# Performance work log

Hardware: AMD Instinct MI355X
Metric: run time of the kernel (lower is better)

The kernel has to match this reference:

```python
import jax, jax.numpy as jnp
import numpy as np
import math

B, S, D, H = 16, 1024, 768, 12
Dh = D // H  # 64


def setup_inputs() -> dict:
    key = jax.random.key(0)
    ks = jax.random.split(key, 9)
    scale = 1.0 / math.sqrt(D)
    X = jax.random.normal(ks[0], (B, S, D), dtype=jnp.float32)
    # Per-head Q/K/V projections stacked along head dim: [H, D, Dh]
    Wq = jax.random.normal(ks[1], (H, D, Dh), dtype=jnp.float32) * scale
    Wk = jax.random.normal(ks[2], (H, D, Dh), dtype=jnp.float32) * scale
    Wv = jax.random.normal(ks[3], (H, D, Dh), dtype=jnp.float32) * scale
    bq = jax.random.normal(ks[4], (H, Dh), dtype=jnp.float32) * scale
    bk = jax.random.normal(ks[5], (H, Dh), dtype=jnp.float32) * scale
    bv = jax.random.normal(ks[6], (H, Dh), dtype=jnp.float32) * scale
    Wo = jax.random.normal(ks[7], (D, D), dtype=jnp.float32) * scale
    bo = jax.random.normal(ks[8], (D,), dtype=jnp.float32) * scale
    return {"X": X, "Wq": Wq, "bq": bq, "Wk": Wk, "bk": bk,
            "Wv": Wv, "bv": bv, "Wo": Wo, "bo": bo}


def reference(X, Wq, bq, Wk, bk, Wv, bv, Wo, bo):
    # Batched multi-head QKV projections (equivalent to the per-head Linear loop).
    Q = jnp.einsum('bsd,hde->bhse', X, Wq) + bq[None, :, None, :]
    K = jnp.einsum('bsd,hde->bhse', X, Wk) + bk[None, :, None, :]
    V = jnp.einsum('bsd,hde->bhse', X, Wv) + bv[None, :, None, :]
    scores = jnp.einsum('bhse,bhte->bhst', Q, K) / jnp.sqrt(jnp.float32(Dh))
    A = jax.nn.softmax(scores, axis=-1)            # [B,H,S,S]
    O = jnp.einsum('bhst,bhte->bhse', A, V)        # [B,H,S,Dh]
    # Concat heads along feature dim (matches torch cat order: head 0 first).
    msa = jnp.transpose(O, (0, 2, 1, 3)).reshape(B, S, D)
    return msa @ Wo + bo
```

## Files before the change

kernel.cpp:

```cpp
#include <hip/hip_runtime.h>
#include <hip/hip_bf16.h>

#define BB 16
#define SS 1024
#define DD 768
#define HH 12
#define DH 64

typedef short short8 __attribute__((ext_vector_type(8)));
typedef float f32x4 __attribute__((ext_vector_type(4)));

__device__ inline float b2f(unsigned short v) {
    union { unsigned int u; float f; } x; x.u = ((unsigned int)v) << 16; return x.f;
}
__device__ inline unsigned short f2b(float f) {
    unsigned int u = __float_as_uint(f);
    u += 0x7FFFu + ((u >> 16) & 1u);
    return (unsigned short)(u >> 16);
}
__device__ inline unsigned int pk2(float a, float b) {
    __hip_bfloat162 h = __float22bfloat162_rn(make_float2(a, b));
    return *(unsigned int*)&h;
}
__device__ inline void cvt8(unsigned short* dst, const float* src) {
    const float4 f0 = *(const float4*)src;
    const float4 f1 = *(const float4*)(src + 4);
    unsigned short t[8] = {f2b(f0.x), f2b(f0.y), f2b(f0.z), f2b(f0.w),
                           f2b(f1.x), f2b(f1.y), f2b(f1.z), f2b(f1.w)};
    *(uint4*)dst = *(const uint4*)t;
}
__device__ __forceinline__ void async16(const void* g, void* l) {
    __builtin_amdgcn_global_load_lds(
        (const __attribute__((address_space(1))) void*)g,
        (__attribute__((address_space(3))) void*)l, 16, 0, 0);
}

__global__ __launch_bounds__(256) void detect_kernel(const unsigned short* __restrict__ X,
                                                     int* __restrict__ flag) {
    __shared__ int s;
    if (threadIdx.x == 0) s = 0;
    __syncthreads();
    int c = 0;
    for (int i = threadIdx.x; i < 16384; i += 256) {
        unsigned short v = X[i];
        if ((v & 0x7FFFu) >= 0x7F80u) c = 1;
    }
    if (c) s = 1;
    __syncthreads();
    if (threadIdx.x == 0) flag[0] = s;
}

__global__ __launch_bounds__(256) void prep_all(
    const void* __restrict__ Xv,
    const void* __restrict__ Wqv, const void* __restrict__ bqv,
    const void* __restrict__ Wkv, const void* __restrict__ bkv,
    const void* __restrict__ Wvv, const void* __restrict__ bvv,
    const void* __restrict__ Wov, const void* __restrict__ bov,
    const int* __restrict__ flag,
    unsigned short* __restrict__ Xb, unsigned short* __restrict__ Wc,
    unsigned short* __restrict__ Wot, unsigned short* __restrict__ bc,
    float* __restrict__ bo32)
{
    __shared__ unsigned short Ls[64][72];
    const int dt = *flag;
    const int u = threadIdx.x;
    const int bx = blockIdx.x;

    if (bx < 6144) {
        size_t base = ((size_t)bx * 256 + u) * 8;
        if (dt) cvt8(Xb + base, (const float*)Xv + base);
        else    *(uint4*)(Xb + base) = *(const uint4*)((const unsigned short*)Xv + base);
        return;
    }
    if (bx < 6720) {
        const int idx = bx - 6144;
        const int kt = idx % 12;
        const int y  = idx / 12;
        const int rk = u >> 2;
        const int e0 = (u & 3) * 16;

        const void* src; size_t srcBase;
        unsigned short* dst; int drow;
        if (y < 36) {
            int z = y / 12, h = y % 12;
            src = (z == 0) ? Wqv : (z == 1) ? Wkv : Wvv;
            srcBase = ((size_t)h * DD + kt * 64 + rk) * DH;
            dst = Wc; drow = z * 768 + h * 64;
        } else {
            int nt = y - 36;
            src = Wov;
            srcBase = (size_t)(kt * 64 + rk) * DD + nt * 64;
            dst = Wot; drow = nt * 64;
        }
#pragma unroll
        for (int ii = 0; ii < 2; ++ii) {
            int e = e0 + ii * 8;
            if (dt) {
                const float* p = (const float*)src + srcBase + e;
                float4 a = *(const float4*)p, b = *(const float4*)(p + 4);
                float v[8] = {a.x, a.y, a.z, a.w, b.x, b.y, b.z, b.w};
#pragma unroll
                for (int j = 0; j < 8; ++j) Ls[e + j][rk] = f2b(v[j]);
            } else {
                union { uint4 v; unsigned short s[8]; } t;
                t.v = *(const uint4*)((const unsigned short*)src + srcBase + e);
#pragma unroll
                for (int j = 0; j < 8; ++j) Ls[e + j][rk] = t.s[j];
            }
        }
        __syncthreads();
        const int e = u >> 2, q = u & 3;
#pragma unroll
        for (int ii = 0; ii < 2; ++ii) {
            int kk = q * 16 + ii * 8;
            *(uint4*)(dst + (size_t)(drow + e) * DD + kt * 64 + kk) = *(const uint4*)(&Ls[e][kk]);
        }
        return;
    }
    for (int n = u; n < 2304; n += 256) {
        int z = n / 768, i = n % 768;
        const void* b = (z == 0) ? bqv : (z == 1) ? bkv : bvv;
        bc[n] = dt ? f2b(((const float*)b)[i]) : ((const unsigned short*)b)[i];
    }
    for (int n = u; n < 768; n += 256)
        bo32[n] = dt ? ((const float*)bov)[n] : b2f(((const unsigned short*)bov)[n]);
}

__global__ __launch_bounds__(256) void qkv_gemm(
    const unsigned short* __restrict__ Xb,
    const unsigned short* __restrict__ Wc,
    const unsigned short* __restrict__ bc,
    unsigned short* __restrict__ Qb, unsigned short* __restrict__ Kb,
    unsigned short* __restrict__ Vtb)
{
    __shared__ __align__(16) unsigned short lds[17408];
    unsigned short* As = lds;
    unsigned short* Bs = lds + 128 * 64;

    const int u = threadIdx.x;
    const int lane = u & 63, w = u >> 6;
    const int ln = lane & 15, quad = lane >> 4;
    const int wm = w & 1, wn = w >> 1;

    const int nt0 = blockIdx.x;
    const int m0  = blockIdx.y << 7;
    const int n0  = nt0 << 7;
    const int z   = nt0 / 6;
    const int hpair = (nt0 % 6) * 2;

    const int rA = w * 32 + (lane >> 3);
    const int c8 = (((lane & 7) ^ (lane >> 3)) * 8);

    f32x4 acc[4][4];
#pragma unroll
    for (int i = 0; i < 4; ++i)
#pragma unroll
        for (int j = 0; j < 4; ++j) acc[i][j] = (f32x4){0.f, 0.f, 0.f, 0.f};

    const unsigned short* Ag = Xb + (size_t)(m0 + rA) * DD + c8;
    const unsigned short* Bg = Wc + (size_t)(n0 + rA) * DD + c8;
    unsigned short* lA0 = As + w * 2048;
    unsigned short* lB0 = Bs + w * 2048;

    for (int kb = 0; kb < 12; ++kb) {
        const int k0 = kb * 64;
        if (kb) __syncthreads();
#pragma unroll
        for (int j = 0; j < 4; ++j) {
            async16(Ag + (size_t)j * 8 * DD + k0, lA0 + j * 512);
            async16(Bg + (size_t)j * 8 * DD + k0, lB0 + j * 512);
        }
        __syncthreads();
#pragma unroll
        for (int kh = 0; kh < 2; ++kh) {
            const int sx = ((kh * 4 + quad) ^ (ln & 7)) * 8;
            short8 af[4], bf[4];
#pragma unroll
            for (int t = 0; t < 4; ++t) {
                af[t] = *(const short8*)(As + (wm * 64 + t * 16 + ln) * 64 + sx);
                bf[t] = *(const short8*)(Bs + (wn * 64 + t * 16 + ln) * 64 + sx);
            }
#pragma unroll
            for (int mt = 0; mt < 4; ++mt)
#pragma unroll
                for (int nt = 0; nt < 4; ++nt)
                    acc[mt][nt] = __builtin_amdgcn_mfma_f32_16x16x32_bf16(af[mt], bf[nt], acc[mt][nt], 0, 0, 0);
        }
    }

    float bias[4];
#pragma unroll
    for (int nt = 0; nt < 4; ++nt) bias[nt] = b2f(bc[n0 + wn * 64 + nt * 16 + ln]);

    const int b = m0 >> 10;
    if (z < 2) {
        unsigned short* O = (z == 0) ? Qb : Kb;
        const float sc = (z == 0) ? 0.180336880111120f : 1.0f;
        const int h = hpair + wn;
        const int sb = (m0 & 1023) + wm * 64;
#pragma unroll
        for (int mt = 0; mt < 4; ++mt)
#pragma unroll
            for (int r = 0; r < 4; ++r) {
                int s = sb + mt * 16 + quad * 4 + r;
                size_t rowo = ((size_t)(b * HH + h) * SS + s) * DH;
#pragma unroll
                for (int nt = 0; nt < 4; ++nt)
                    O[rowo + nt * 16 + ln] = f2b((acc[mt][nt][r] + bias[nt]) * sc);
            }
    } else {
        __syncthreads();
#pragma unroll
        for (int mt = 0; mt < 4; ++mt)
#pragma unroll
            for (int nt = 0; nt < 4; ++nt)
#pragma unroll
                for (int r = 0; r < 4; ++r)
                    lds[(wn * 64 + nt * 16 + ln) * 136 + wm * 64 + mt * 16 + quad * 4 + r] =
                        f2b(acc[mt][nt][r] + bias[nt]);
        __syncthreads();
        const int cc = u >> 1, half = u & 1;
        const int h = hpair + (cc >> 6), e = cc & 63;
        const int sb = (m0 & 1023) + half * 64;
        unsigned short* dst = Vtb + ((size_t)(b * HH + h) * DH + e) * SS + sb;
        const unsigned short* srcp = lds + cc * 136 + half * 64;
#pragma unroll
        for (int i = 0; i < 8; ++i)
            *(uint4*)(dst + i * 8) = *(const uint4*)(srcp + i * 8);
    }
}

__global__ __launch_bounds__(256, 6) void attn_kernel(
    const unsigned short* __restrict__ Kb,
    const unsigned short* __restrict__ Vtb,
    unsigned short* __restrict__ Qb)
{
    __shared__ __align__(16) unsigned short QPs[64][72];
    __shared__ __align__(16) unsigned short Ks[4096];
    __shared__ __align__(16) unsigned short Vs[4096];

    const int u = threadIdx.x;
    const int s0 = blockIdx.x << 6;
    const int bh = blockIdx.y;

    const int lane = u & 63, w = u >> 6;
    const int ln = lane & 15, quad = lane >> 4;

    unsigned short* Qg = Qb + ((size_t)bh * SS + s0) * DH;
    const unsigned short* Kg = Kb + (size_t)bh * SS * DH;
    const unsigned short* Vg = Vtb + (size_t)bh * DH * SS;

    const int xrow = u >> 3, xch = u & 7;
#pragma unroll
    for (int p = 0; p < 2; ++p) {
        int r2 = xrow + 32 * p;
        *(uint4*)(&QPs[r2][xch * 8]) = *(const uint4*)(Qg + r2 * DH + xch * 8);
    }
    __syncthreads();
    short8 qf0 = *(const short8*)(&QPs[16 * w + ln][quad * 8]);
    short8 qf1 = *(const short8*)(&QPs[16 * w + ln][32 + quad * 8]);

    short8 ones;
#pragma unroll
    for (int i = 0; i < 8; ++i) ones[i] = (short)0x3F80;

    f32x4 acc_o[4];
#pragma unroll
    for (int i = 0; i < 4; ++i) acc_o[i] = (f32x4){0.f, 0.f, 0.f, 0.f};
    f32x4 acc_l = (f32x4){0.f, 0.f, 0.f, 0.f};

    const int srow = lane >> 3;
    const int cg8  = ((lane & 7) ^ srow) * 8;
    const unsigned short* kp0 = Kg + (size_t)((w * 2 + 0) * 8 + srow) * DH + cg8;
    const unsigned short* kp1 = Kg + (size_t)((w * 2 + 1) * 8 + srow) * DH + cg8;
    const unsigned short* vp0 = Vg + (size_t)((w * 2 + 0) * 8 + srow) * SS + cg8;
    const unsigned short* vp1 = Vg + (size_t)((w * 2 + 1) * 8 + srow) * SS + cg8;
    unsigned short* lk0 = Ks + (w * 2 + 0) * 512;
    unsigned short* lk1 = Ks + (w * 2 + 1) * 512;
    unsigned short* lv0 = Vs + (w * 2 + 0) * 512;
    unsigned short* lv1 = Vs + (w * 2 + 1) * 512;

    const unsigned short* kb0 = Ks + ln * 64 + ((quad) ^ (ln & 7)) * 8;
    const unsigned short* kb1 = Ks + ln * 64 + ((4 + quad) ^ (ln & 7)) * 8;
    const unsigned short* vb0 = Vs + ln * 64 + ((quad) ^ (ln & 7)) * 8;
    const unsigned short* vb1 = Vs + ln * 64 + ((4 + quad) ^ (ln & 7)) * 8;
    unsigned short* psw = &QPs[16 * w + ln][quad * 4];
    const unsigned short* psr0 = &QPs[16 * w + ln][quad * 8];
    const unsigned short* psr1 = &QPs[16 * w + ln][32 + quad * 8];

    for (int kt = 0; kt < 16; ++kt) {
        __syncthreads();
        async16(kp0, lk0); async16(kp1, lk1);
        async16(vp0, lv0); async16(vp1, lv1);
        kp0 += 64 * DH; kp1 += 64 * DH; vp0 += 64; vp1 += 64;
        __syncthreads();

        f32x4 acc_s[4];
#pragma unroll
        for (int nt = 0; nt < 4; ++nt) {
            short8 kf0 = *(const short8*)(kb0 + nt * 1024);
            short8 kf1 = *(const short8*)(kb1 + nt * 1024);
            f32x4 zz = (f32x4){0.f, 0.f, 0.f, 0.f};
            zz = __builtin_amdgcn_mfma_f32_16x16x32_bf16(kf0, qf0, zz, 0, 0, 0);
            zz = __builtin_amdgcn_mfma_f32_16x16x32_bf16(kf1, qf1, zz, 0, 0, 0);
            acc_s[nt] = zz;
        }

#pragma unroll
        for (int nt = 0; nt < 4; ++nt) {
            uint2 pw;
            pw.x = pk2(exp2f(acc_s[nt][0]), exp2f(acc_s[nt][1]));
            pw.y = pk2(exp2f(acc_s[nt][2]), exp2f(acc_s[nt][3]));
            *(uint2*)(psw + nt * 16) = pw;
        }

        short8 pf0 = *(const short8*)psr0;
        short8 pf1 = *(const short8*)psr1;
        acc_l = __builtin_amdgcn_mfma_f32_16x16x32_bf16(pf0, ones, acc_l, 0, 0, 0);
        acc_l = __builtin_amdgcn_mfma_f32_16x16x32_bf16(pf1, ones, acc_l, 0, 0, 0);
#pragma unroll
        for (int nt = 0; nt < 4; ++nt) {
            short8 vf0 = *(const short8*)(vb0 + nt * 1024);
            short8 vf1 = *(const short8*)(vb1 + nt * 1024);
            acc_o[nt] = __builtin_amdgcn_mfma_f32_16x16x32_bf16(pf0, vf0, acc_o[nt], 0, 0, 0);
            acc_o[nt] = __builtin_amdgcn_mfma_f32_16x16x32_bf16(pf1, vf1, acc_o[nt], 0, 0, 0);
        }
    }

    float inv[4];
#pragma unroll
    for (int r = 0; r < 4; ++r) inv[r] = 1.f / acc_l[r];
#pragma unroll
    for (int nt = 0; nt < 4; ++nt)
#pragma unroll
        for (int r = 0; r < 4; ++r) {
            int row = 16 * w + quad * 4 + r;
            Qg[row * DH + nt * 16 + ln] = f2b(acc_o[nt][r] * inv[r]);
        }
}

__global__ __launch_bounds__(256) void oproj_gemm(
    const unsigned short* __restrict__ Ob,
    const unsigned short* __restrict__ Wot,
    const float* __restrict__ bo32,
    float* __restrict__ out)
{
    __shared__ __align__(16) unsigned short lds[128 * 128];
    unsigned short* As = lds;
    unsigned short* Bs = lds + 128 * 64;

    const int u = threadIdx.x;
    const int lane = u & 63, w = u >> 6;
    const int ln = lane & 15, quad = lane >> 4;
    const int wm = w & 1, wn = w >> 1;

    const int n0 = blockIdx.x << 7;
    const int m0 = blockIdx.y << 7;
    const int b = m0 >> 10, s0t = m0 & 1023;

    const int rA = w * 32 + (lane >> 3);
    const int c8 = (((lane & 7) ^ (lane >> 3)) * 8);

    f32x4 acc[4][4];
#pragma unroll
    for (int i = 0; i < 4; ++i)
#pragma unroll
        for (int j = 0; j < 4; ++j) acc[i][j] = (f32x4){0.f, 0.f, 0.f, 0.f};

    const unsigned short* Bg = Wot + (size_t)(n0 + rA) * DD + c8;
    unsigned short* lA0 = As + w * 2048;
    unsigned short* lB0 = Bs + w * 2048;

    for (int kb = 0; kb < 12; ++kb) {
        if (kb) __syncthreads();
        const unsigned short* Ag = Ob + ((size_t)(b * HH + kb) * SS + s0t + rA) * DH + c8;
#pragma unroll
        for (int j = 0; j < 4; ++j) {
            async16(Ag + (size_t)j * 8 * DH, lA0 + j * 512);
            async16(Bg + (size_t)j * 8 * DD + kb * 64, lB0 + j * 512);
        }
        __syncthreads();
#pragma unroll
        for (int kh = 0; kh < 2; ++kh) {
            const int sx = ((kh * 4 + quad) ^ (ln & 7)) * 8;
            short8 af[4], bf[4];
#pragma unroll
            for (int t = 0; t < 4; ++t) {
                af[t] = *(const short8*)(As + (wm * 64 + t * 16 + ln) * 64 + sx);
                bf[t] = *(const short8*)(Bs + (wn * 64 + t * 16 + ln) * 64 + sx);
            }
#pragma unroll
            for (int mt = 0; mt < 4; ++mt)
#pragma unroll
                for (int nt = 0; nt < 4; ++nt)
                    acc[mt][nt] = __builtin_amdgcn_mfma_f32_16x16x32_bf16(af[mt], bf[nt], acc[mt][nt], 0, 0, 0);
        }
    }

    float bias[4];
#pragma unroll
    for (int nt = 0; nt < 4; ++nt) bias[nt] = bo32[n0 + wn * 64 + nt * 16 + ln];
#pragma unroll
    for (int mt = 0; mt < 4; ++mt)
#pragma unroll
        for (int r = 0; r < 4; ++r) {
            int m = m0 + wm * 64 + mt * 16 + quad * 4 + r;
            float* orow = out + (size_t)m * DD + n0 + wn * 64;
#pragma unroll
            for (int nt = 0; nt < 4; ++nt)
                orow[nt * 16 + ln] = acc[mt][nt][r] + bias[nt];
        }
}

extern "C" void kernel_launch(void* const* d_in, const int* in_sizes, int n_in,
                              void* d_out, int out_size, void* d_ws, size_t ws_size,
                              hipStream_t stream)
{
    const void* X  = d_in[0];
    const void* Wq = d_in[1];
    const void* bq = d_in[2];
    const void* Wk = d_in[3];
    const void* bk = d_in[4];
    const void* Wv = d_in[5];
    const void* bv = d_in[6];
    const void* Wo = d_in[7];
    const void* bo = d_in[8];
    float* out = (float*)d_out;

    const size_t NE = (size_t)BB * HH * SS * DH;
    char* p = (char*)d_ws;
    int* flag = (int*)p;                 p += 256;
    unsigned short* Qb  = (unsigned short*)p;  p += NE * 2;
    unsigned short* Kb  = (unsigned short*)p;  p += NE * 2;
    unsigned short* Vtb = (unsigned short*)p;  p += NE * 2;
    unsigned short* Xb  = (unsigned short*)p;  p += (size_t)BB * SS * DD * 2;
    unsigned short* Wc  = (unsigned short*)p;  p += (size_t)3 * DD * DD * 2;
    unsigned short* Wot = (unsigned short*)p;  p += (size_t)DD * DD * 2;
    unsigned short* bcb = (unsigned short*)p;  p += 4608;
    float* bo32 = (float*)p;                   p += 3072;

    detect_kernel<<<1, 256, 0, stream>>>((const unsigned short*)X, flag);
    prep_all<<<6721, 256, 0, stream>>>(X, Wq, bq, Wk, bk, Wv, bv, Wo, bo, flag,
                                       Xb, Wc, Wot, bcb, bo32);
    qkv_gemm<<<dim3(18, 128), 256, 0, stream>>>(Xb, Wc, bcb, Qb, Kb, Vtb);
    attn_kernel<<<dim3(16, 192), 256, 0, stream>>>(Kb, Vtb, Qb);
    oproj_gemm<<<dim3(6, 128), 256, 0, stream>>>(Qb, Wot, bo32, out);
}
```

Measured before the change: 326.2 us.

## Process 128 query rows per attention block to reuse K/V tiles

The attention kernel now handles 128 query rows per block (two 64-row sub-blocks per wave) instead of 64, halving the grid and halving K/V tile loads per query. Q is loaded with async global-to-LDS copies into a swizzled layout, P is written back through the same swizzle, and exp2f is replaced with the hardware exp2 builtin. The cost is more registers and LDS per block, with the occupancy hint lowered from 6 to 4 and fewer blocks in flight.

```diff
diff --git a/kernel.cpp b/kernel.cpp
--- a/kernel.cpp
+++ b/kernel.cpp
@@ -21,6 +21,13 @@
 __device__ inline unsigned int pk2(float a, float b) {
     __hip_bfloat162 h = __float22bfloat162_rn(make_float2(a, b));
     return *(unsigned int*)&h;
+}
+__device__ __forceinline__ float fast_exp2(float x) {
+#if __has_builtin(__builtin_amdgcn_exp2f)
+    return __builtin_amdgcn_exp2f(x);
+#else
+    return exp2f(x);
+#endif
 }
 __device__ inline void cvt8(unsigned short* dst, const float* src) {
     const float4 f0 = *(const float4*)src;
@@ -230,17 +237,17 @@
     }
 }
 
-__global__ __launch_bounds__(256, 6) void attn_kernel(
+__global__ __launch_bounds__(256, 4) void attn_kernel(
     const unsigned short* __restrict__ Kb,
     const unsigned short* __restrict__ Vtb,
     unsigned short* __restrict__ Qb)
 {
-    __shared__ __align__(16) unsigned short QPs[64][72];
+    __shared__ __align__(16) unsigned short QPs[8192];
     __shared__ __align__(16) unsigned short Ks[4096];
     __shared__ __align__(16) unsigned short Vs[4096];
 
     const int u = threadIdx.x;
-    const int s0 = blockIdx.x << 6;
+    const int s0 = blockIdx.x << 7;
     const int bh = blockIdx.y;
 
     const int lane = u & 63, w = u >> 6;
@@ -250,27 +257,38 @@
     const unsigned short* Kg = Kb + (size_t)bh * SS * DH;
     const unsigned short* Vg = Vtb + (size_t)bh * DH * SS;
 
-    const int xrow = u >> 3, xch = u & 7;
-#pragma unroll
-    for (int p = 0; p < 2; ++p) {
-        int r2 = xrow + 32 * p;
-        *(uint4*)(&QPs[r2][xch * 8]) = *(const uint4*)(Qg + r2 * DH + xch * 8);
-    }
-    __syncthreads();
-    short8 qf0 = *(const short8*)(&QPs[16 * w + ln][quad * 8]);
-    short8 qf1 = *(const short8*)(&QPs[16 * w + ln][32 + quad * 8]);
-
-    short8 ones;
-#pragma unroll
-    for (int i = 0; i < 8; ++i) ones[i] = (short)0x3F80;
-
-    f32x4 acc_o[4];
-#pragma unroll
-    for (int i = 0; i < 4; ++i) acc_o[i] = (f32x4){0.f, 0.f, 0.f, 0.f};
-    f32x4 acc_l = (f32x4){0.f, 0.f, 0.f, 0.f};
-
     const int srow = lane >> 3;
     const int cg8  = ((lane & 7) ^ srow) * 8;
+
+#pragma unroll
+    for (int j = 0; j < 4; ++j) {
+        const int r0 = (w * 4 + j) * 8 + srow;
+        async16(Qg + (size_t)r0 * DH + cg8, QPs + (w * 4 + j) * 512);
+    }
+    __syncthreads();
+
+    short8 qf[2][2];
+#pragma unroll
+    for (int b = 0; b < 2; ++b) {
+        const int rb = b * 64 + 16 * w + ln;
+#pragma unroll
+        for (int kh = 0; kh < 2; ++kh)
+            qf[b][kh] = *(const short8*)(QPs + rb * 64 + ((kh * 4 + quad) ^ (ln & 7)) * 8);
+    }
+
+    short8 ones;
+#pragma unroll
+    for (int i = 0; i < 8; ++i) ones[i] = (short)0x3F80;
+
+    f32x4 acc_o[2][4];
+#pragma unroll
+    for (int b = 0; b < 2; ++b)
+#pragma unroll
+        for (int i = 0; i < 4; ++i) acc_o[b][i] = (f32x4){0.f, 0.f, 0.f, 0.f};
+    f32x4 acc_l[2];
+    acc_l[0] = (f32x4){0.f, 0.f, 0.f, 0.f};
+    acc_l[1] = (f32x4){0.f, 0.f, 0.f, 0.f};
+
     const unsigned short* kp0 = Kg + (size_t)((w * 2 + 0) * 8 + srow) * DH + cg8;
     const unsigned short* kp1 = Kg + (size_t)((w * 2 + 1) * 8 + srow) * DH + cg8;
     const unsigned short* vp0 = Vg + (size_t)((w * 2 + 0) * 8 + srow) * SS + cg8;
@@ -280,13 +298,10 @@
     unsigned short* lv0 = Vs + (w * 2 + 0) * 512;
     unsigned short* lv1 = Vs + (w * 2 + 1) * 512;
 
-    const unsigned short* kb0 = Ks + ln * 64 + ((quad) ^ (ln & 7)) * 8;
-    const unsigned short* kb1 = Ks + ln * 64 + ((4 + quad) ^ (ln & 7)) * 8;
-    const unsigned short* vb0 = Vs + ln * 64 + ((quad) ^ (ln & 7)) * 8;
-    const unsigned short* vb1 = Vs + ln * 64 + ((4 + quad) ^ (ln & 7)) * 8;
-    unsigned short* psw = &QPs[16 * w + ln][quad * 4];
-    const unsigned short* psr0 = &QPs[16 * w + ln][quad * 8];
-    const unsigned short* psr1 = &QPs[16 * w + ln][32 + quad * 8];
+    const unsigned short* kb0 = Ks + ln * 64 + ((quad ^ (ln & 7)) * 8);
+    const unsigned short* kb1 = Ks + ln * 64 + (((4 + quad) ^ (ln & 7)) * 8);
+    const unsigned short* vb0 = Vs + ln * 64 + ((quad ^ (ln & 7)) * 8);
+    const unsigned short* vb1 = Vs + ln * 64 + (((4 + quad) ^ (ln & 7)) * 8);
 
     for (int kt = 0; kt < 16; ++kt) {
         __syncthreads();
@@ -295,48 +310,67 @@
         kp0 += 64 * DH; kp1 += 64 * DH; vp0 += 64; vp1 += 64;
         __syncthreads();
 
-        f32x4 acc_s[4];
+        f32x4 acc_s[2][4];
 #pragma unroll
         for (int nt = 0; nt < 4; ++nt) {
             short8 kf0 = *(const short8*)(kb0 + nt * 1024);
             short8 kf1 = *(const short8*)(kb1 + nt * 1024);
-            f32x4 zz = (f32x4){0.f, 0.f, 0.f, 0.f};
-            zz = __builtin_amdgcn_mfma_f32_16x16x32_bf16(kf0, qf0, zz, 0, 0, 0);
-            zz = __builtin_amdgcn_mfma_f32_16x16x32_bf16(kf1, qf1, zz, 0, 0, 0);
-            acc_s[nt] = zz;
-        }
-
-#pragma unroll
-        for (int nt = 0; nt < 4; ++nt) {
-            uint2 pw;
-            pw.x = pk2(exp2f(acc_s[nt][0]), exp2f(acc_s[nt][1]));
-            pw.y = pk2(exp2f(acc_s[nt][2]), exp2f(acc_s[nt][3]));
-            *(uint2*)(psw + nt * 16) = pw;
-        }
-
-        short8 pf0 = *(const short8*)psr0;
-        short8 pf1 = *(const short8*)psr1;
-        acc_l = __builtin_amdgcn_mfma_f32_16x16x32_bf16(pf0, ones, acc_l, 0, 0, 0);
-        acc_l = __builtin_amdgcn_mfma_f32_16x16x32_bf16(pf1, ones, acc_l, 0, 0, 0);
+#pragma unroll
+            for (int b = 0; b < 2; ++b) {
+                f32x4 zz = (f32x4){0.f, 0.f, 0.f, 0.f};
+                zz = __builtin_amdgcn_mfma_f32_16x16x32_bf16(kf0, qf[b][0], zz, 0, 0, 0);
+                zz = __builtin_amdgcn_mfma_f32_16x16x32_bf16(kf1, qf[b][1], zz, 0, 0, 0);
+                acc_s[b][nt] = zz;
+            }
+        }
+
+#pragma unroll
+        for (int b = 0; b < 2; ++b) {
+            unsigned short* pb = QPs + (b * 64 + 16 * w + ln) * 64 + (quad & 1) * 4;
+#pragma unroll
+            for (int nt = 0; nt < 4; ++nt) {
+                uint2 pw;
+                pw.x = pk2(fast_exp2(acc_s[b][nt][0]), fast_exp2(acc_s[b][nt][1]));
+                pw.y = pk2(fast_exp2(acc_s[b][nt][2]), fast_exp2(acc_s[b][nt][3]));
+                const int c = (nt * 2 + (quad >> 1)) ^ (ln & 7);
+                *(uint2*)(pb + c * 8) = pw;
+            }
+        }
+
+        short8 pf[2][2];
+#pragma unroll
+        for (int b = 0; b < 2; ++b) {
+            const unsigned short* pr = QPs + (b * 64 + 16 * w + ln) * 64;
+            pf[b][0] = *(const short8*)(pr + ((quad ^ (ln & 7)) * 8));
+            pf[b][1] = *(const short8*)(pr + (((4 + quad) ^ (ln & 7)) * 8));
+            acc_l[b] = __builtin_amdgcn_mfma_f32_16x16x32_bf16(pf[b][0], ones, acc_l[b], 0, 0, 0);
+            acc_l[b] = __builtin_amdgcn_mfma_f32_16x16x32_bf16(pf[b][1], ones, acc_l[b], 0, 0, 0);
+        }
 #pragma unroll
         for (int nt = 0; nt < 4; ++nt) {
             short8 vf0 = *(const short8*)(vb0 + nt * 1024);
             short8 vf1 = *(const short8*)(vb1 + nt * 1024);
-            acc_o[nt] = __builtin_amdgcn_mfma_f32_16x16x32_bf16(pf0, vf0, acc_o[nt], 0, 0, 0);
-            acc_o[nt] = __builtin_amdgcn_mfma_f32_16x16x32_bf16(pf1, vf1, acc_o[nt], 0, 0, 0);
-        }
-    }
-
-    float inv[4];
-#pragma unroll
-    for (int r = 0; r < 4; ++r) inv[r] = 1.f / acc_l[r];
-#pragma unroll
-    for (int nt = 0; nt < 4; ++nt)
-#pragma unroll
-        for (int r = 0; r < 4; ++r) {
-            int row = 16 * w + quad * 4 + r;
-            Qg[row * DH + nt * 16 + ln] = f2b(acc_o[nt][r] * inv[r]);
-        }
+#pragma unroll
+            for (int b = 0; b < 2; ++b) {
+                acc_o[b][nt] = __builtin_amdgcn_mfma_f32_16x16x32_bf16(pf[b][0], vf0, acc_o[b][nt], 0, 0, 0);
+                acc_o[b][nt] = __builtin_amdgcn_mfma_f32_16x16x32_bf16(pf[b][1], vf1, acc_o[b][nt], 0, 0, 0);
+            }
+        }
+    }
+
+#pragma unroll
+    for (int b = 0; b < 2; ++b) {
+        float inv[4];
+#pragma unroll
+        for (int r = 0; r < 4; ++r) inv[r] = 1.f / acc_l[b][r];
+#pragma unroll
+        for (int nt = 0; nt < 4; ++nt)
+#pragma unroll
+            for (int r = 0; r < 4; ++r) {
+                int row = b * 64 + 16 * w + quad * 4 + r;
+                Qg[row * DH + nt * 16 + ln] = f2b(acc_o[b][nt][r] * inv[r]);
+            }
+    }
 }
 
 __global__ __launch_bounds__(256) void oproj_gemm(
@@ -443,6 +477,6 @@
     prep_all<<<6721, 256, 0, stream>>>(X, Wq, bq, Wk, bk, Wv, bv, Wo, bo, flag,
                                        Xb, Wc, Wot, bcb, bo32);
     qkv_gemm<<<dim3(18, 128), 256, 0, stream>>>(Xb, Wc, bcb, Qb, Kb, Vtb);
-    attn_kernel<<<dim3(16, 192), 256, 0, stream>>>(Kb, Vtb, Qb);
+    attn_kernel<<<dim3(8, 192), 256, 0, stream>>>(Kb, Vtb, Qb);
     oproj_gemm<<<dim3(6, 128), 256, 0, stream>>>(Qb, Wot, bo32, out);
 }
```

Measured after the change: 304.8 us. -6.6%, faster.
